# Kernel optimization log

Hardware: AMD Instinct MI355X
Metric: run time of the kernel (lower is better)

The kernel has to match this reference:

```python
import jax, jax.numpy as jnp
import numpy as np

N_U, N_I, D = 30000, 15000, 64
L = 2                 # propagation layers (self.l)
TEMP = 0.2
LAMBDA1, LAMBDA2 = 0.2, 1e-7
H, F = 4, 16          # GAT heads x per-head dim; H*F == D
NEG_SLOPE = 0.2
AVG_DEG = 16
B = 2048


def setup_inputs() -> dict:
    key = jax.random.key(0)
    ks = jax.random.split(key, 10)
    rng = np.random.default_rng(0)
    E_u_0 = jax.random.normal(ks[0], (N_U, D), jnp.float32) * 0.1
    E_i_0 = jax.random.normal(ks[1], (N_I, D), jnp.float32) * 0.1
    # sparse normalized bipartite adjacency (adj_norm) as an edge list
    nnz = N_U * AVG_DEG
    u_idx = np.repeat(np.arange(N_U), AVG_DEG)
    i_idx = rng.integers(0, N_I, nnz)
    deg_u = np.bincount(u_idx, minlength=N_U)
    deg_i = np.maximum(np.bincount(i_idx, minlength=N_I), 1)
    vals = (1.0 / np.sqrt(deg_u[u_idx] * deg_i[i_idx])).astype(np.float32)
    # GAT graph on n_u+n_i nodes: bipartite edges both directions + self-loops
    n = N_U + N_I
    src = np.concatenate([u_idx, i_idx + N_U, np.arange(n)]).astype(np.int32)
    dst = np.concatenate([i_idx + N_U, u_idx, np.arange(n)]).astype(np.int32)
    # GAT parameters (fresh each forward in original, so just random)
    W = jax.random.normal(ks[2], (D, H * F), jnp.float32) / np.sqrt(D)
    attn_l = jax.random.normal(ks[3], (H, F), jnp.float32) * 0.1
    attn_r = jax.random.normal(ks[4], (H, F), jnp.float32) * 0.1
    uids = jax.random.randint(ks[5], (B,), 0, N_U, jnp.int32)
    iids = jax.random.randint(ks[6], (B,), 0, N_I, jnp.int32)
    pos = jax.random.randint(ks[7], (B,), 0, N_I, jnp.int32)
    neg = jax.random.randint(ks[8], (B,), 0, N_I, jnp.int32)
    return dict(E_u_0=E_u_0, E_i_0=E_i_0, adj_vals=jnp.asarray(vals),
                W=W, attn_l=attn_l, attn_r=attn_r,
                u_idx=jnp.asarray(u_idx, jnp.int32), i_idx=jnp.asarray(i_idx, jnp.int32),
                src=jnp.asarray(src), dst=jnp.asarray(dst),
                uids=uids, iids=iids, pos=pos, neg=neg)


def gat_layer(h, src, dst, W, attn_l, attn_r, n_nodes):
    # GATConv: project, per-edge attention, neighborhood softmax, scatter-agg
    feat = (h @ W).reshape(-1, H, F)                      # [N,H,F]
    el = (feat * attn_l).sum(-1)                          # [N,H]
    er = (feat * attn_r).sum(-1)                          # [N,H]
    e = jax.nn.leaky_relu(el[src] + er[dst], NEG_SLOPE)   # [E,H]
    e_max = jax.ops.segment_max(e, dst, num_segments=n_nodes)
    a = jnp.exp(e - e_max[dst])
    denom = jax.ops.segment_sum(a, dst, num_segments=n_nodes)
    a = a / denom[dst]                                    # self-loops => denom>0
    out = jax.ops.segment_sum(a[:, :, None] * feat[src], dst, num_segments=n_nodes)
    return jax.nn.elu(out.reshape(-1, H * F))             # [N,D]


def _forward(E_u_0, E_i_0, adj_vals, W, attn_l, attn_r,
             u_idx, i_idx, src, dst, uids, iids, pos, neg):
    n = N_U + N_I
    Eu, Ei = E_u_0, E_i_0
    sum_Eu, sum_Ei = E_u_0, E_i_0
    sum_Gu, sum_Gi = E_u_0, E_i_0
    for _ in range(L):
        # LightGCN spmm propagation: Z_u = A @ E_i, Z_i = A.T @ E_u
        Zu = jax.ops.segment_sum(adj_vals[:, None] * Ei[i_idx], u_idx, num_segments=N_U)
        Zi = jax.ops.segment_sum(adj_vals[:, None] * Eu[u_idx], i_idx, num_segments=N_I)
        ls1 = gat_layer(jnp.concatenate([Eu, Ei], 0), src, dst, W, attn_l, attn_r, n)
        Gu, Gi = ls1[:N_U], ls1[N_U:]
        Eu, Ei = Zu + Eu, Zi + Ei
        sum_Eu = sum_Eu + Eu
        sum_Ei = sum_Ei + Ei
        sum_Gu = sum_Gu + Gu
        sum_Gi = sum_Gi + Gi
    log_eps = jnp.float32(np.log(1e-8))
    # InfoNCE: log(sum(exp(s)) + 1e-8) == logaddexp(logsumexp(s), log(1e-8))
    lse_u = jax.scipy.special.logsumexp(sum_Gu[uids] @ sum_Eu.T / TEMP, axis=1)
    lse_i = jax.scipy.special.logsumexp(sum_Gi[iids] @ sum_Ei.T / TEMP, axis=1)
    neg_score = jnp.logaddexp(lse_u, log_eps).mean() + jnp.logaddexp(lse_i, log_eps).mean()
    pos_score = ((sum_Gu[uids] * sum_Eu[uids]).sum(1) / TEMP).mean() \
              + ((sum_Gi[iids] * sum_Ei[iids]).sum(1) / TEMP).mean()
    loss_s = -pos_score + neg_score
    # BPR loss
    u_emb = sum_Eu[uids]
    diff = (u_emb * sum_Ei[pos]).sum(-1) - (u_emb * sum_Ei[neg]).sum(-1)
    loss_r = -jax.nn.log_sigmoid(diff).mean()
    # L2 reg over nn.Parameters (E_u_0, E_i_0 only)
    loss_reg = LAMBDA2 * ((E_u_0 ** 2).sum() + (E_i_0 ** 2).sum())
    loss = loss_r + LAMBDA1 * loss_s + loss_reg
    return loss, loss_r, LAMBDA1 * loss_s


def reference(E_u_0, E_i_0, adj_vals, W, attn_l, attn_r,
              u_idx, i_idx, src, dst, uids, iids, pos, neg):
    return _forward(E_u_0, E_i_0, adj_vals, W, attn_l, attn_r,
                    u_idx, i_idx, src, dst, uids, iids, pos, neg)
```

## Files before the change

### kernel.cpp

```cpp
#include <hip/hip_runtime.h>
#include <math.h>

#define N_U 30000
#define N_I 15000
#define N_TOT 45000
#define D 64
#define NNZ 480000
#define B 2048
#define INV_TEMP 5.0f
#define LOG_EPS -18.420680743952367f
#define NEG_SLOPE 0.2f
#define LAMBDA1 0.2f
#define LAMBDA2 1e-7f

#define NSP 128
#define RSP_U 235
#define RSP_I 118
#define PAD_U 30016
#define PAD_I 15040
#define SCALE_LOG2 7.2134752044448170f
#define LN2F 0.6931471805599453f

typedef __attribute__((ext_vector_type(8))) short short8;
typedef __attribute__((ext_vector_type(4))) float f32x4;

__device__ inline float wred(float v) {
#pragma unroll
  for (int o = 32; o > 0; o >>= 1) v += __shfl_down(v, o, 64);
  return v;
}

__device__ inline float leaky(float v) { return (v >= 0.f) ? v : NEG_SLOPE * v; }

__device__ inline void atomMaxF(float* a, float v) {
  if (v >= 0.f) atomicMax((int*)a, __float_as_int(v));
  else atomicMin((unsigned int*)a, __float_as_uint(v));
}

__device__ inline unsigned short f2bf(float x) {
  unsigned u = __float_as_uint(x);
  unsigned r = u + 0x7FFFu + ((u >> 16) & 1u);
  return (unsigned short)(r >> 16);
}
__device__ inline float bf2f(unsigned short h) {
  return __uint_as_float(((unsigned)h) << 16);
}

__global__ void k_init(const float* __restrict__ Eu0, const float* __restrict__ Ei0,
                       float* fU, float* fI,
                       unsigned short* gU, unsigned short* gI,
                       float* sEu, float* sEi,
                       float* sGu, float* sGi, int* deg, float* acc) {
  int t = blockIdx.x * 256 + threadIdx.x;
  if (t < 20) acc[t] = (t >= 8 && t < 16) ? -INFINITY : 0.f;
  if (t < N_I) deg[t] = 0;
  int n = t >> 4, q = t & 15;
  if (n < N_U) {
    float4 v = ((const float4*)Eu0)[t];
    ((float4*)(fU + (size_t)n * 128))[q] = v;
    ushort4 bv = {f2bf(v.x), f2bf(v.y), f2bf(v.z), f2bf(v.w)};
    ((ushort4*)(gU + (size_t)n * 128))[q] = bv;
    ((float4*)sEu)[t] = v;
    ((float4*)sGu)[t] = v;
  } else if (n < N_TOT) {
    int j = t - N_U * 16;
    int ni = n - N_U;
    float4 v = ((const float4*)Ei0)[j];
    ((float4*)(fI + (size_t)ni * 128))[q] = v;
    ushort4 bv = {f2bf(v.x), f2bf(v.y), f2bf(v.z), f2bf(v.w)};
    ((ushort4*)(gI + (size_t)ni * 128))[q] = bv;
    ((float4*)sEi)[j] = v;
    ((float4*)sGi)[j] = v;
  }
}

__global__ void k_deg(const int* __restrict__ ii, int* deg) {
  int e = blockIdx.x * 256 + threadIdx.x;
  if (e < NNZ) atomicAdd(&deg[ii[e]], 1);
}

__global__ void k_scan(const int* __restrict__ deg, int* rowptr, int* cursor) {
  __shared__ int wtot[16], woff[16];
  const int CHUNK = 15;
  int tid = threadIdx.x, lane = tid & 63, wv = tid >> 6;
  int base = tid * CHUNK;
  int dv[CHUNK];
  int s = 0;
#pragma unroll
  for (int k = 0; k < CHUNK; k++) {
    int idx = base + k;
    dv[k] = (idx < N_I) ? deg[idx] : 0;
    s += dv[k];
  }
  int v = s;
#pragma unroll
  for (int o = 1; o < 64; o <<= 1) {
    int x = __shfl_up(v, o, 64);
    if (lane >= o) v += x;
  }
  if (lane == 63) wtot[wv] = v;
  __syncthreads();
  if (tid < 16) {
    int w = wtot[tid];
    int iv = w;
#pragma unroll
    for (int o = 1; o < 16; o <<= 1) {
      int x = __shfl_up(iv, o, 16);
      if (tid >= o) iv += x;
    }
    woff[tid] = iv - w;
  }
  __syncthreads();
  int excl = (v - s) + woff[wv];
#pragma unroll
  for (int k = 0; k < CHUNK; k++) {
    int idx = base + k;
    if (idx < N_I) {
      rowptr[idx] = excl;
      cursor[idx] = excl;
      excl += dv[k];
    }
  }
  if (tid == 1023) rowptr[N_I] = excl;
}

__global__ void k_fill(const int* __restrict__ ii, const float* __restrict__ vals,
                       int* cursor, int* u_srt, float* v_srt) {
  int e = blockIdx.x * 256 + threadIdx.x;
  if (e < NNZ) {
    int pos = atomicAdd(&cursor[ii[e]], 1);
    u_srt[pos] = e >> 4;
    v_srt[pos] = vals[e];
  }
}

__global__ void k_feat(float* __restrict__ fU, float* __restrict__ fI,
                       unsigned short* __restrict__ gU, unsigned short* __restrict__ gI,
                       const float* __restrict__ W, const float* __restrict__ al,
                       const float* __restrict__ ar,
                       float* __restrict__ el, float* __restrict__ er) {
  __shared__ float Ws[64 * 64];
  __shared__ float hs[16][64];
  int tid = threadIdx.x;
  for (int t = tid; t < 1024; t += 256) ((float4*)Ws)[t] = ((const float4*)W)[t];
  int g = tid >> 6, c = tid & 63;
  int n0 = blockIdx.x * 16 + g * 4;
  float* rows[4];
  unsigned short* grows[4];
#pragma unroll
  for (int j = 0; j < 4; j++) {
    int node = n0 + j;
    rows[j] = nullptr; grows[j] = nullptr;
    if (node < N_TOT) {
      if (node < N_U) {
        rows[j] = fU + (size_t)node * 128;
        grows[j] = gU + (size_t)node * 128;
      } else {
        rows[j] = fI + (size_t)(node - N_U) * 128;
        grows[j] = gI + (size_t)(node - N_U) * 128;
      }
      hs[g * 4 + j][c] = rows[j][c];
    }
  }
  __syncthreads();
  float a0 = 0.f, a1 = 0.f, a2 = 0.f, a3 = 0.f;
#pragma unroll 8
  for (int k = 0; k < 64; ++k) {
    float w = Ws[k * 64 + c];
    a0 = fmaf(hs[g * 4 + 0][k], w, a0);
    a1 = fmaf(hs[g * 4 + 1][k], w, a1);
    a2 = fmaf(hs[g * 4 + 2][k], w, a2);
    a3 = fmaf(hs[g * 4 + 3][k], w, a3);
  }
  float accs[4] = {a0, a1, a2, a3};
  float alc = al[c], arc = ar[c];
#pragma unroll
  for (int j = 0; j < 4; j++) {
    int node = n0 + j;
    if (node >= N_TOT) continue;
    rows[j][64 + c] = accs[j];
    grows[j][64 + c] = f2bf(accs[j]);
    float pl = accs[j] * alc;
    float pr = accs[j] * arc;
#pragma unroll
    for (int o = 8; o >= 1; o >>= 1) {
      pl += __shfl_down(pl, o, 16);
      pr += __shfl_down(pr, o, 16);
    }
    if ((c & 15) == 0) {
      el[node * 4 + (c >> 4)] = pl;
      er[node * 4 + (c >> 4)] = pr;
    }
  }
}

__global__ void k_elmax(const float* __restrict__ el, float* __restrict__ dst) {
  __shared__ float red[4][4];
  int tid = threadIdx.x;
  int lane = tid & 63, wv = tid >> 6;
  float mx = -INFINITY;
  for (int t = blockIdx.x * 256 + tid; t < N_TOT * 4; t += 64 * 256)
    mx = fmaxf(mx, el[t]);
#pragma unroll
  for (int o = 4; o < 64; o <<= 1) mx = fmaxf(mx, __shfl_xor(mx, o, 64));
  if (lane < 4) red[wv][lane] = mx;
  __syncthreads();
  if (tid < 4) {
    float m2 = fmaxf(fmaxf(red[0][tid], red[1][tid]), fmaxf(red[2][tid], red[3][tid]));
    atomMaxF(dst + tid, m2);
  }
}

__global__ void k_layer(const float* __restrict__ fU_cur, const float* __restrict__ fI_cur,
                        const unsigned short* __restrict__ gU_cur,
                        const unsigned short* __restrict__ gI_cur,
                        const float* __restrict__ el, const float* __restrict__ er,
                        const float* __restrict__ vals, const int* __restrict__ ii,
                        const int* __restrict__ rowptr, const int* __restrict__ u_srt,
                        const float* __restrict__ v_srt,
                        const float* __restrict__ elmx,
                        float* __restrict__ fU_nxt, float* __restrict__ fI_nxt,
                        unsigned short* __restrict__ gU_nxt, unsigned short* __restrict__ gI_nxt,
                        float* __restrict__ sEu, float* __restrict__ sEi,
                        float* __restrict__ sGu, float* __restrict__ sGi,
                        unsigned short* __restrict__ EuH, unsigned short* __restrict__ EuL,
                        unsigned short* __restrict__ EiH, unsigned short* __restrict__ EiL,
                        float* __restrict__ normU, float* __restrict__ normI) {
  int t = blockIdx.x * 256 + threadIdx.x;
  int node = t >> 6, c = t & 63;
  if (node >= N_TOT) return;
  int h = c >> 4;

  if (node < N_U) {
    int u = node;
    float eru = er[u * 4 + h];
    float m = leaky(elmx[h] + eru);
    const float* selfrow = fU_cur + (size_t)u * 128;
    float aself = __expf(leaky(el[u * 4 + h] + eru) - m);

    int idx[16]; float vv[16];
#pragma unroll
    for (int k = 0; k < 16; k++) { idx[k] = ii[u * 16 + k]; vv[k] = vals[u * 16 + k]; }
    float av[16];
#pragma unroll
    for (int k = 0; k < 16; k++)
      av[k] = __expf(leaky(el[(idx[k] + N_U) * 4 + h] + eru) - m);

    float den = aself;
#pragma unroll
    for (int k = 0; k < 16; k++) den += av[k];

    float o0 = aself * selfrow[64 + c], o1 = 0.f;
    float z0 = 0.f, z1 = 0.f;
#pragma unroll
    for (int k = 0; k < 16; k += 2) {
      const unsigned short* rA = gI_cur + (size_t)idx[k] * 128;
      const unsigned short* rB = gI_cur + (size_t)idx[k + 1] * 128;
      float eA = bf2f(rA[c]), fA = bf2f(rA[64 + c]);
      float eB = bf2f(rB[c]), fB = bf2f(rB[64 + c]);
      z0 = fmaf(vv[k], eA, z0);
      z1 = fmaf(vv[k + 1], eB, z1);
      o0 = fmaf(av[k], fA, o0);
      o1 = fmaf(av[k + 1], fB, o1);
    }
    float o = (o0 + o1) / den;
    float g = (o > 0.f) ? o : expm1f(o);
    float e_new = selfrow[c] + z0 + z1;
    fU_nxt[(size_t)u * 128 + c] = e_new;
    gU_nxt[(size_t)u * 128 + c] = f2bf(e_new);
    size_t off = (size_t)u * D + c;
    float s_final = sEu[off] + e_new;
    sEu[off] = s_final;
    sGu[off] += g;
    if (EuH) {
      unsigned short hi = f2bf(s_final);
      EuH[off] = hi;
      EuL[off] = f2bf(s_final - bf2f(hi));
      float n2 = wred(s_final * s_final);
      if (c == 0) normU[u] = n2;
    }
  } else {
    int i = node - N_U;
    float eri = er[node * 4 + h];
    float m = leaky(elmx[h] + eri);
    const float* selfrow = fI_cur + (size_t)i * 128;
    float aself = __expf(leaky(el[node * 4 + h] + eri) - m);
    float den0 = aself, den1 = 0.f;
    float o0 = aself * selfrow[64 + c], o1 = 0.f;
    float z0 = 0.f, z1 = 0.f;
    int r0 = rowptr[i], r1 = rowptr[i + 1];
    int r = r0;
    for (; r + 3 < r1; r += 4) {
      int u0 = u_srt[r], u1 = u_srt[r + 1], u2 = u_srt[r + 2], u3 = u_srt[r + 3];
      float v0 = v_srt[r], v1 = v_srt[r + 1], v2 = v_srt[r + 2], v3 = v_srt[r + 3];
      float a0 = __expf(leaky(el[u0 * 4 + h] + eri) - m);
      float a1 = __expf(leaky(el[u1 * 4 + h] + eri) - m);
      float a2 = __expf(leaky(el[u2 * 4 + h] + eri) - m);
      float a3 = __expf(leaky(el[u3 * 4 + h] + eri) - m);
      const unsigned short* R0 = gU_cur + (size_t)u0 * 128;
      const unsigned short* R1 = gU_cur + (size_t)u1 * 128;
      const unsigned short* R2 = gU_cur + (size_t)u2 * 128;
      const unsigned short* R3 = gU_cur + (size_t)u3 * 128;
      float e0 = bf2f(R0[c]), f0 = bf2f(R0[64 + c]);
      float e1 = bf2f(R1[c]), f1 = bf2f(R1[64 + c]);
      float e2 = bf2f(R2[c]), f2 = bf2f(R2[64 + c]);
      float e3 = bf2f(R3[c]), f3 = bf2f(R3[64 + c]);
      z0 = fmaf(v0, e0, z0); z1 = fmaf(v1, e1, z1);
      z0 = fmaf(v2, e2, z0); z1 = fmaf(v3, e3, z1);
      den0 += a0 + a2; den1 += a1 + a3;
      o0 = fmaf(a0, f0, o0); o1 = fmaf(a1, f1, o1);
      o0 = fmaf(a2, f2, o0); o1 = fmaf(a3, f3, o1);
    }
    for (; r < r1; r++) {
      int u0 = u_srt[r];
      float v0 = v_srt[r];
      float a0 = __expf(leaky(el[u0 * 4 + h] + eri) - m);
      const unsigned short* R0 = gU_cur + (size_t)u0 * 128;
      float e0 = bf2f(R0[c]), f0 = bf2f(R0[64 + c]);
      z0 = fmaf(v0, e0, z0);
      den0 += a0;
      o0 = fmaf(a0, f0, o0);
    }
    float o = (o0 + o1) / (den0 + den1);
    float g = (o > 0.f) ? o : expm1f(o);
    float e_new = selfrow[c] + z0 + z1;
    fI_nxt[(size_t)i * 128 + c] = e_new;
    gI_nxt[(size_t)i * 128 + c] = f2bf(e_new);
    size_t off = (size_t)i * D + c;
    float s_final = sEi[off] + e_new;
    sEi[off] = s_final;
    sGi[off] += g;
    if (EiH) {
      unsigned short hi = f2bf(s_final);
      EiH[off] = hi;
      EiL[off] = f2bf(s_final - bf2f(hi));
      float n2 = wred(s_final * s_final);
      if (c == 0) normI[i] = n2;
    }
  }
}

__global__ void k_normreg(const float* __restrict__ nU, const float* __restrict__ nI,
                          const float* __restrict__ Eu0, const float* __restrict__ Ei0,
                          float* __restrict__ acc) {
  __shared__ float red[4][3];
  int tid = threadIdx.x;
  int lane = tid & 63, wv = tid >> 6;
  float mu = 0.f, mi = 0.f, s = 0.f;
  for (int t = blockIdx.x * 256 + tid; t < N_U; t += 128 * 256) mu = fmaxf(mu, nU[t]);
  for (int t = blockIdx.x * 256 + tid; t < N_I; t += 128 * 256) mi = fmaxf(mi, nI[t]);
  const float4* A = (const float4*)Eu0;
  const float4* Bp = (const float4*)Ei0;
  const int nA = N_U * 16, nTot = N_TOT * 16;
  for (int t = blockIdx.x * 256 + tid; t < nTot; t += 128 * 256) {
    float4 v = (t < nA) ? A[t] : Bp[t - nA];
    s += v.x * v.x + v.y * v.y + v.z * v.z + v.w * v.w;
  }
#pragma unroll
  for (int o = 32; o > 0; o >>= 1) {
    mu = fmaxf(mu, __shfl_down(mu, o, 64));
    mi = fmaxf(mi, __shfl_down(mi, o, 64));
    s += __shfl_down(s, o, 64);
  }
  if (lane == 0) { red[wv][0] = mu; red[wv][1] = mi; red[wv][2] = s; }
  __syncthreads();
  if (tid == 0) {
    float a = fmaxf(fmaxf(red[0][0], red[1][0]), fmaxf(red[2][0], red[3][0]));
    float b = fmaxf(fmaxf(red[0][1], red[1][1]), fmaxf(red[2][1], red[3][1]));
    float ssum = red[0][2] + red[1][2] + red[2][2] + red[3][2];
    atomMaxF(acc + 6, a);
    atomMaxF(acc + 7, b);
    unsafeAtomicAdd(acc + 5, ssum);
  }
}

__global__ void k_cvt_q(const float* __restrict__ sGu, const float* __restrict__ sGi,
                        const int* __restrict__ uids, const int* __restrict__ iids,
                        unsigned short* __restrict__ QuH, unsigned short* __restrict__ QuL,
                        unsigned short* __restrict__ QiH, unsigned short* __restrict__ QiL,
                        const float* __restrict__ acc,
                        float* __restrict__ M0u, float* __restrict__ M0i) {
  int lane = threadIdx.x & 63, wv = threadIdx.x >> 6;
  int row = blockIdx.x * 4 + wv;
  int side = row >> 11;
  int b = row & (B - 1);
  int id = side ? iids[b] : uids[b];
  float x = (side ? sGi : sGu)[(size_t)id * 64 + lane] * SCALE_LOG2;
  unsigned short hi = f2bf(x);
  unsigned short lo = f2bf(x - bf2f(hi));
  if (side) { QiH[(size_t)b * 64 + lane] = hi; QiL[(size_t)b * 64 + lane] = lo; }
  else      { QuH[(size_t)b * 64 + lane] = hi; QuL[(size_t)b * 64 + lane] = lo; }
  float n2 = wred(x * x);
  if (lane == 0) {
    float en2 = side ? acc[7] : acc[6];
    float M0 = sqrtf(n2) * sqrtf(en2) * 1.01f + 1.0f;
    (side ? M0i : M0u)[b] = M0;
  }
}

__global__ __launch_bounds__(256, 2) void k_lse_mfma(
    const unsigned short* __restrict__ QuH, const unsigned short* __restrict__ QuL,
    const unsigned short* __restrict__ EuHp, const unsigned short* __restrict__ EuLp,
    const unsigned short* __restrict__ QiH, const unsigned short* __restrict__ QiL,
    const unsigned short* __restrict__ EiHp, const unsigned short* __restrict__ EiLp,
    const float* __restrict__ M0u, const float* __restrict__ M0i,
    float* __restrict__ psU, float* __restrict__ psI) {
  int z = blockIdx.z;
  const unsigned short* Qhi = z ? QiH : QuH;
  const unsigned short* Qlo = z ? QiL : QuL;
  const unsigned short* Ehi = z ? EiHp : EuHp;
  const unsigned short* Elo = z ? EiLp : EuLp;
  const float* M0arr = z ? M0i : M0u;
  float* part_s = z ? psI : psU;
  int n_rows = z ? N_I : N_U;
  int rows_per_split = z ? RSP_I : RSP_U;

  int tid = threadIdx.x;
  int wave = tid >> 6, lane = tid & 63;
  int l15 = lane & 15, quad = lane >> 4;
  int qbase = (blockIdx.x * 4 + wave) * 128;
  int split = blockIdx.y;
  int row0 = split * rows_per_split;
  int row_end = min(row0 + rows_per_split, n_rows);
  int rows = row_end - row0; if (rows < 0) rows = 0;
  int total = (rows + 15) >> 4;
  int ntail = rows & 15;

  float ss[8][4];
#pragma unroll
  for (int t = 0; t < 8; t++)
#pragma unroll
    for (int g = 0; g < 4; g++) ss[t][g] = 0.f;

  if (total > 0) {
    short8 ah[8][2], al[8][2];
#pragma unroll
    for (int t = 0; t < 8; t++)
#pragma unroll
      for (int c = 0; c < 2; c++) {
        size_t idx = (size_t)(qbase + t * 16 + l15) * 64 + c * 32 + quad * 8;
        ah[t][c] = *(const short8*)(Qhi + idx);
        al[t][c] = *(const short8*)(Qlo + idx);
      }

    f32x4 cinit[8];
#pragma unroll
    for (int t = 0; t < 8; t++)
#pragma unroll
      for (int g = 0; g < 4; g++)
        cinit[t][g] = -M0arr[qbase + t * 16 + quad * 4 + g];

    const unsigned short* ph = Ehi + (size_t)(row0 + l15) * 64 + quad * 8;
    const unsigned short* pl = Elo + (size_t)(row0 + l15) * 64 + quad * 8;

    short8 cb0 = *(const short8*)(ph);
    short8 cb1 = *(const short8*)(ph + 32);
    short8 cb2 = *(const short8*)(pl);
    short8 cb3 = *(const short8*)(pl + 32);
    ph += 1024; pl += 1024;

    for (int it = 0; it < total - 1; it++) {
      short8 nb0 = *(const short8*)(ph);
      short8 nb1 = *(const short8*)(ph + 32);
      short8 nb2 = *(const short8*)(pl);
      short8 nb3 = *(const short8*)(pl + 32);
      ph += 1024; pl += 1024;
#pragma unroll
      for (int t = 0; t < 8; t++) {
        f32x4 acc = cinit[t];
        acc = __builtin_amdgcn_mfma_f32_16x16x32_bf16(ah[t][0], cb0, acc, 0, 0, 0);
        acc = __builtin_amdgcn_mfma_f32_16x16x32_bf16(ah[t][1], cb1, acc, 0, 0, 0);
        acc = __builtin_amdgcn_mfma_f32_16x16x32_bf16(al[t][0], cb0, acc, 0, 0, 0);
        acc = __builtin_amdgcn_mfma_f32_16x16x32_bf16(al[t][1], cb1, acc, 0, 0, 0);
        acc = __builtin_amdgcn_mfma_f32_16x16x32_bf16(ah[t][0], cb2, acc, 0, 0, 0);
        acc = __builtin_amdgcn_mfma_f32_16x16x32_bf16(ah[t][1], cb3, acc, 0, 0, 0);
#pragma unroll
        for (int g = 0; g < 4; g++)
          ss[t][g] += exp2f(acc[g]);
      }
      cb0 = nb0; cb1 = nb1; cb2 = nb2; cb3 = nb3;
    }
    {
      bool valid = (ntail == 0) || (l15 < ntail);
#pragma unroll
      for (int t = 0; t < 8; t++) {
        f32x4 acc = cinit[t];
        acc = __builtin_amdgcn_mfma_f32_16x16x32_bf16(ah[t][0], cb0, acc, 0, 0, 0);
        acc = __builtin_amdgcn_mfma_f32_16x16x32_bf16(ah[t][1], cb1, acc, 0, 0, 0);
        acc = __builtin_amdgcn_mfma_f32_16x16x32_bf16(al[t][0], cb0, acc, 0, 0, 0);
        acc = __builtin_amdgcn_mfma_f32_16x16x32_bf16(al[t][1], cb1, acc, 0, 0, 0);
        acc = __builtin_amdgcn_mfma_f32_16x16x32_bf16(ah[t][0], cb2, acc, 0, 0, 0);
        acc = __builtin_amdgcn_mfma_f32_16x16x32_bf16(ah[t][1], cb3, acc, 0, 0, 0);
#pragma unroll
        for (int g = 0; g < 4; g++) {
          float e = exp2f(acc[g]);
          ss[t][g] += valid ? e : 0.f;
        }
      }
    }
  }

#pragma unroll
  for (int off = 1; off < 16; off <<= 1) {
#pragma unroll
    for (int t = 0; t < 8; t++)
#pragma unroll
      for (int g = 0; g < 4; g++)
        ss[t][g] += __shfl_xor(ss[t][g], off, 64);
  }

  if (l15 == 0) {
#pragma unroll
    for (int t = 0; t < 8; t++)
#pragma unroll
      for (int g = 0; g < 4; g++) {
        int q = qbase + t * 16 + quad * 4 + g;
        part_s[(size_t)split * B + q] = ss[t][g];
      }
  }
}

__global__ void k_small(const float* __restrict__ sEu, const float* __restrict__ sEi,
                        const float* __restrict__ sGu, const float* __restrict__ sGi,
                        const int* __restrict__ uids, const int* __restrict__ iids,
                        const int* __restrict__ pos, const int* __restrict__ neg,
                        const float* __restrict__ psU, const float* __restrict__ psI,
                        const float* __restrict__ M0u, const float* __restrict__ M0i,
                        float* acc, float* __restrict__ out) {
  int b = blockIdx.x * 256 + threadIdx.x;
  float du = 0.f, di = 0.f, nu = 0.f, ni = 0.f, bpr = 0.f;
  if (b < B) {
    float su = 0.f, si = 0.f;
    for (int s2 = 0; s2 < NSP; s2++) su += psU[(size_t)s2 * B + b];
    for (int s2 = 0; s2 < NSP; s2++) si += psI[(size_t)s2 * B + b];
    float lseu = M0u[b] * LN2F + logf(su);
    float lsei = M0i[b] * LN2F + logf(si);
    nu = fmaxf(lseu, LOG_EPS) + log1pf(expf(-fabsf(lseu - LOG_EPS)));
    ni = fmaxf(lsei, LOG_EPS) + log1pf(expf(-fabsf(lsei - LOG_EPS)));

    int u = uids[b], it = iids[b], p = pos[b], ng = neg[b];
    const float4* gu = (const float4*)(sGu + (size_t)u * D);
    const float4* eu = (const float4*)(sEu + (size_t)u * D);
    const float4* gi = (const float4*)(sGi + (size_t)it * D);
    const float4* ei = (const float4*)(sEi + (size_t)it * D);
    const float4* ep = (const float4*)(sEi + (size_t)p * D);
    const float4* en = (const float4*)(sEi + (size_t)ng * D);
    float diff = 0.f;
#pragma unroll
    for (int k = 0; k < 16; k++) {
      float4 a = gu[k], b4 = eu[k];
      du += a.x * b4.x + a.y * b4.y + a.z * b4.z + a.w * b4.w;
      float4 c = gi[k], d4 = ei[k];
      di += c.x * d4.x + c.y * d4.y + c.z * d4.z + c.w * d4.w;
      float4 e = ep[k], f = en[k];
      diff += b4.x * (e.x - f.x) + b4.y * (e.y - f.y) + b4.z * (e.z - f.z) + b4.w * (e.w - f.w);
    }
    bpr = (diff > 0.f) ? log1pf(expf(-diff)) : (-diff + log1pf(expf(diff)));
  }
  du = wred(du); di = wred(di); nu = wred(nu); ni = wred(ni); bpr = wred(bpr);
  if ((threadIdx.x & 63) == 0) {
    unsafeAtomicAdd(acc + 0, du);
    unsafeAtomicAdd(acc + 1, di);
    unsafeAtomicAdd(acc + 2, nu);
    unsafeAtomicAdd(acc + 3, ni);
    unsafeAtomicAdd(acc + 4, bpr);
  }
  __syncthreads();
  if (threadIdx.x == 0) {
    __threadfence();
    int ticket = atomicAdd((int*)(acc + 16), 1);
    if (ticket == (int)gridDim.x - 1) {
      __threadfence();
      float a0 = unsafeAtomicAdd(acc + 0, 0.f);
      float a1 = unsafeAtomicAdd(acc + 1, 0.f);
      float a2 = unsafeAtomicAdd(acc + 2, 0.f);
      float a3 = unsafeAtomicAdd(acc + 3, 0.f);
      float a4 = unsafeAtomicAdd(acc + 4, 0.f);
      float a5 = unsafeAtomicAdd(acc + 5, 0.f);
      float pos_score = (a0 + a1) * (INV_TEMP / (float)B);
      float neg_score = (a2 + a3) / (float)B;
      float loss_s = neg_score - pos_score;
      float loss_r = a4 / (float)B;
      float reg = LAMBDA2 * a5;
      out[0] = loss_r + LAMBDA1 * loss_s + reg;
      out[1] = loss_r;
      out[2] = LAMBDA1 * loss_s;
    }
  }
}

extern "C" void kernel_launch(void* const* d_in, const int* in_sizes, int n_in,
                              void* d_out, int out_size, void* d_ws, size_t ws_size,
                              hipStream_t stream) {
  const float* Eu0  = (const float*)d_in[0];
  const float* Ei0  = (const float*)d_in[1];
  const float* vals = (const float*)d_in[2];
  const float* W    = (const float*)d_in[3];
  const float* al   = (const float*)d_in[4];
  const float* ar   = (const float*)d_in[5];
  const int* ii     = (const int*)d_in[7];
  const int* uids   = (const int*)d_in[10];
  const int* iids   = (const int*)d_in[11];
  const int* pos    = (const int*)d_in[12];
  const int* neg    = (const int*)d_in[13];
  float* out = (float*)d_out;

  char* base = (char*)d_ws;
  size_t off = 0;
  auto alloc = [&](size_t bytes) -> void* {
    void* p = base + off;
    off = (off + bytes + 255) & ~(size_t)255;
    return p;
  };
  float* fU_a = (float*)alloc((size_t)N_U * 128 * 4);
  float* fU_b = (float*)alloc((size_t)N_U * 128 * 4);
  float* fI_a = (float*)alloc((size_t)N_I * 128 * 4);
  float* fI_b = (float*)alloc((size_t)N_I * 128 * 4);
  unsigned short* gU_a = (unsigned short*)alloc((size_t)N_U * 128 * 2);
  unsigned short* gU_b = (unsigned short*)alloc((size_t)N_U * 128 * 2);
  unsigned short* gI_a = (unsigned short*)alloc((size_t)N_I * 128 * 2);
  unsigned short* gI_b = (unsigned short*)alloc((size_t)N_I * 128 * 2);
  float* sEu  = (float*)alloc((size_t)N_U * D * 4);
  float* sEi  = (float*)alloc((size_t)N_I * D * 4);
  float* sGu  = (float*)alloc((size_t)N_U * D * 4);
  float* sGi  = (float*)alloc((size_t)N_I * D * 4);
  float* el   = (float*)alloc((size_t)N_TOT * 4 * 4);
  float* er   = (float*)alloc((size_t)N_TOT * 4 * 4);
  float* psU  = (float*)alloc((size_t)B * NSP * 4);
  float* psI  = (float*)alloc((size_t)B * NSP * 4);
  float* M0u  = (float*)alloc((size_t)B * 4);
  float* M0i  = (float*)alloc((size_t)B * 4);
  float* normU= (float*)alloc((size_t)N_U * 4);
  float* normI= (float*)alloc((size_t)N_I * 4);
  float* acc  = (float*)alloc(32 * 4);
  int* deg    = (int*)alloc((size_t)N_I * 4);
  int* cursor = (int*)alloc((size_t)N_I * 4);
  int* rowptr = (int*)alloc((size_t)(N_I + 1) * 4);
  int* u_srt  = (int*)alloc((size_t)NNZ * 4);
  float* v_srt= (float*)alloc((size_t)NNZ * 4);
  unsigned short* EuH = (unsigned short*)alloc((size_t)PAD_U * 64 * 2);
  unsigned short* EuL = (unsigned short*)alloc((size_t)PAD_U * 64 * 2);
  unsigned short* EiH = (unsigned short*)alloc((size_t)PAD_I * 64 * 2);
  unsigned short* EiL = (unsigned short*)alloc((size_t)PAD_I * 64 * 2);
  unsigned short* QuH = (unsigned short*)alloc((size_t)B * 64 * 2);
  unsigned short* QuL = (unsigned short*)alloc((size_t)B * 64 * 2);
  unsigned short* QiH = (unsigned short*)alloc((size_t)B * 64 * 2);
  unsigned short* QiL = (unsigned short*)alloc((size_t)B * 64 * 2);

  k_init<<<(N_TOT * 16 + 255) / 256, 256, 0, stream>>>(Eu0, Ei0, fU_a, fI_a, gU_a, gI_a,
                                                       sEu, sEi, sGu, sGi, deg, acc);
  k_deg<<<(NNZ + 255) / 256, 256, 0, stream>>>(ii, deg);
  k_scan<<<1, 1024, 0, stream>>>(deg, rowptr, cursor);
  k_fill<<<(NNZ + 255) / 256, 256, 0, stream>>>(ii, vals, cursor, u_srt, v_srt);

  float* cu = fU_a; float* ci = fI_a;
  float* nu = fU_b; float* ni = fI_b;
  unsigned short* gcu = gU_a; unsigned short* gci = gI_a;
  unsigned short* gnu = gU_b; unsigned short* gni = gI_b;
  for (int l = 0; l < 2; ++l) {
    float* elmx = acc + 8 + 4 * l;
    bool last = (l == 1);
    k_feat<<<(N_TOT + 15) / 16, 256, 0, stream>>>(cu, ci, gcu, gci, W, al, ar, el, er);
    k_elmax<<<64, 256, 0, stream>>>(el, elmx);
    k_layer<<<(N_TOT * D) / 256, 256, 0, stream>>>(
        cu, ci, gcu, gci, el, er, vals, ii, rowptr, u_srt, v_srt, elmx,
        nu, ni, gnu, gni, sEu, sEi, sGu, sGi,
        last ? EuH : nullptr, last ? EuL : nullptr,
        last ? EiH : nullptr, last ? EiL : nullptr,
        normU, normI);
    float* t1 = cu; cu = nu; nu = t1;
    float* t2 = ci; ci = ni; ni = t2;
    unsigned short* t3 = gcu; gcu = gnu; gnu = t3;
    unsigned short* t4 = gci; gci = gni; gni = t4;
  }

  k_normreg<<<128, 256, 0, stream>>>(normU, normI, Eu0, Ei0, acc);
  k_cvt_q<<<(2 * B) / 4, 256, 0, stream>>>(sGu, sGi, uids, iids, QuH, QuL, QiH, QiL, acc, M0u, M0i);
  k_lse_mfma<<<dim3(B / 512, NSP, 2), 256, 0, stream>>>(QuH, QuL, EuH, EuL,
                                                        QiH, QiL, EiH, EiL,
                                                        M0u, M0i, psU, psI);
  k_small<<<B / 256, 256, 0, stream>>>(sEu, sEi, sGu, sGi, uids, iids, pos, neg,
                                       psU, psI, M0u, M0i, acc, out);
}
```

Baseline: 424.7 us.

## Interleave bf16 embedding/feature pairs and compute attention exps once per lane with shuffles

Changes the bf16 gather buffers so that the embedding and the projected GAT feature for each channel sit next to each other, letting one 32-bit load fetch both instead of two 16-bit loads from separate halves of the row. Each lane in a 16-lane head group now computes the attention exp for one neighbour and shares it with the others through wave shuffles, rather than every lane recomputing all 16 exps. The item path is restructured into 16-edge chunks to fit the shuffle scheme. This adds shuffle traffic and a layout dependency between the init, projection and propagate kernels.

After: 409.5 us. 3.6% less time.

```diff
diff --git a/kernel.cpp b/kernel.cpp
--- a/kernel.cpp
+++ b/kernel.cpp
@@ -58,8 +58,8 @@
   if (n < N_U) {
     float4 v = ((const float4*)Eu0)[t];
     ((float4*)(fU + (size_t)n * 128))[q] = v;
-    ushort4 bv = {f2bf(v.x), f2bf(v.y), f2bf(v.z), f2bf(v.w)};
-    ((ushort4*)(gU + (size_t)n * 128))[q] = bv;
+    uint4 gv = {(unsigned)f2bf(v.x), (unsigned)f2bf(v.y), (unsigned)f2bf(v.z), (unsigned)f2bf(v.w)};
+    ((uint4*)(gU + (size_t)n * 128))[q] = gv;
     ((float4*)sEu)[t] = v;
     ((float4*)sGu)[t] = v;
   } else if (n < N_TOT) {
@@ -67,8 +67,8 @@
     int ni = n - N_U;
     float4 v = ((const float4*)Ei0)[j];
     ((float4*)(fI + (size_t)ni * 128))[q] = v;
-    ushort4 bv = {f2bf(v.x), f2bf(v.y), f2bf(v.z), f2bf(v.w)};
-    ((ushort4*)(gI + (size_t)ni * 128))[q] = bv;
+    uint4 gv = {(unsigned)f2bf(v.x), (unsigned)f2bf(v.y), (unsigned)f2bf(v.z), (unsigned)f2bf(v.w)};
+    ((uint4*)(gI + (size_t)ni * 128))[q] = gv;
     ((float4*)sEi)[j] = v;
     ((float4*)sGi)[j] = v;
   }
@@ -179,7 +179,7 @@
     int node = n0 + j;
     if (node >= N_TOT) continue;
     rows[j][64 + c] = accs[j];
-    grows[j][64 + c] = f2bf(accs[j]);
+    grows[j][2 * c + 1] = f2bf(accs[j]);
     float pl = accs[j] * alc;
     float pr = accs[j] * arc;
 #pragma unroll
@@ -230,6 +230,7 @@
   int node = t >> 6, c = t & 63;
   if (node >= N_TOT) return;
   int h = c >> 4;
+  int k2 = c & 15;
 
   if (node < N_U) {
     int u = node;
@@ -241,10 +242,12 @@
     int idx[16]; float vv[16];
 #pragma unroll
     for (int k = 0; k < 16; k++) { idx[k] = ii[u * 16 + k]; vv[k] = vals[u * 16 + k]; }
+
+    float ev = __expf(leaky(el[(ii[u * 16 + k2] + N_U) * 4 + h] + eru) - m);
     float av[16];
 #pragma unroll
     for (int k = 0; k < 16; k++)
-      av[k] = __expf(leaky(el[(idx[k] + N_U) * 4 + h] + eru) - m);
+      av[k] = __shfl(ev, (c & 48) | k, 64);
 
     float den = aself;
 #pragma unroll
@@ -254,10 +257,10 @@
     float z0 = 0.f, z1 = 0.f;
 #pragma unroll
     for (int k = 0; k < 16; k += 2) {
-      const unsigned short* rA = gI_cur + (size_t)idx[k] * 128;
-      const unsigned short* rB = gI_cur + (size_t)idx[k + 1] * 128;
-      float eA = bf2f(rA[c]), fA = bf2f(rA[64 + c]);
-      float eB = bf2f(rB[c]), fB = bf2f(rB[64 + c]);
+      unsigned wA = *(const unsigned*)(gI_cur + (size_t)idx[k] * 128 + 2 * c);
+      unsigned wB = *(const unsigned*)(gI_cur + (size_t)idx[k + 1] * 128 + 2 * c);
+      float eA = __uint_as_float(wA << 16), fA = __uint_as_float(wA & 0xFFFF0000u);
+      float eB = __uint_as_float(wB << 16), fB = __uint_as_float(wB & 0xFFFF0000u);
       z0 = fmaf(vv[k], eA, z0);
       z1 = fmaf(vv[k + 1], eB, z1);
       o0 = fmaf(av[k], fA, o0);
@@ -267,7 +270,7 @@
     float g = (o > 0.f) ? o : expm1f(o);
     float e_new = selfrow[c] + z0 + z1;
     fU_nxt[(size_t)u * 128 + c] = e_new;
-    gU_nxt[(size_t)u * 128 + c] = f2bf(e_new);
+    gU_nxt[(size_t)u * 128 + 2 * c] = f2bf(e_new);
     size_t off = (size_t)u * D + c;
     float s_final = sEu[off] + e_new;
     sEu[off] = s_final;
@@ -289,43 +292,48 @@
     float o0 = aself * selfrow[64 + c], o1 = 0.f;
     float z0 = 0.f, z1 = 0.f;
     int r0 = rowptr[i], r1 = rowptr[i + 1];
-    int r = r0;
-    for (; r + 3 < r1; r += 4) {
-      int u0 = u_srt[r], u1 = u_srt[r + 1], u2 = u_srt[r + 2], u3 = u_srt[r + 3];
-      float v0 = v_srt[r], v1 = v_srt[r + 1], v2 = v_srt[r + 2], v3 = v_srt[r + 3];
-      float a0 = __expf(leaky(el[u0 * 4 + h] + eri) - m);
-      float a1 = __expf(leaky(el[u1 * 4 + h] + eri) - m);
-      float a2 = __expf(leaky(el[u2 * 4 + h] + eri) - m);
-      float a3 = __expf(leaky(el[u3 * 4 + h] + eri) - m);
-      const unsigned short* R0 = gU_cur + (size_t)u0 * 128;
-      const unsigned short* R1 = gU_cur + (size_t)u1 * 128;
-      const unsigned short* R2 = gU_cur + (size_t)u2 * 128;
-      const unsigned short* R3 = gU_cur + (size_t)u3 * 128;
-      float e0 = bf2f(R0[c]), f0 = bf2f(R0[64 + c]);
-      float e1 = bf2f(R1[c]), f1 = bf2f(R1[64 + c]);
-      float e2 = bf2f(R2[c]), f2 = bf2f(R2[64 + c]);
-      float e3 = bf2f(R3[c]), f3 = bf2f(R3[64 + c]);
-      z0 = fmaf(v0, e0, z0); z1 = fmaf(v1, e1, z1);
-      z0 = fmaf(v2, e2, z0); z1 = fmaf(v3, e3, z1);
-      den0 += a0 + a2; den1 += a1 + a3;
-      o0 = fmaf(a0, f0, o0); o1 = fmaf(a1, f1, o1);
-      o0 = fmaf(a2, f2, o0); o1 = fmaf(a3, f3, o1);
-    }
-    for (; r < r1; r++) {
-      int u0 = u_srt[r];
-      float v0 = v_srt[r];
-      float a0 = __expf(leaky(el[u0 * 4 + h] + eri) - m);
-      const unsigned short* R0 = gU_cur + (size_t)u0 * 128;
-      float e0 = bf2f(R0[c]), f0 = bf2f(R0[64 + c]);
-      z0 = fmaf(v0, e0, z0);
-      den0 += a0;
-      o0 = fmaf(a0, f0, o0);
+    for (int rb = r0; rb < r1; rb += 16) {
+      int cnt = min(16, r1 - rb);
+      int rr = rb + (k2 < cnt ? k2 : cnt - 1);
+      float ev = __expf(leaky(el[u_srt[rr] * 4 + h] + eri) - m);
+      int k = 0;
+      for (; k + 3 < cnt; k += 4) {
+        int u0 = u_srt[rb + k], u1 = u_srt[rb + k + 1], u2 = u_srt[rb + k + 2], u3 = u_srt[rb + k + 3];
+        float v0 = v_srt[rb + k], v1 = v_srt[rb + k + 1], v2 = v_srt[rb + k + 2], v3 = v_srt[rb + k + 3];
+        float a0 = __shfl(ev, (c & 48) | k, 64);
+        float a1 = __shfl(ev, (c & 48) | (k + 1), 64);
+        float a2 = __shfl(ev, (c & 48) | (k + 2), 64);
+        float a3 = __shfl(ev, (c & 48) | (k + 3), 64);
+        unsigned w0 = *(const unsigned*)(gU_cur + (size_t)u0 * 128 + 2 * c);
+        unsigned w1 = *(const unsigned*)(gU_cur + (size_t)u1 * 128 + 2 * c);
+        unsigned w2 = *(const unsigned*)(gU_cur + (size_t)u2 * 128 + 2 * c);
+        unsigned w3 = *(const unsigned*)(gU_cur + (size_t)u3 * 128 + 2 * c);
+        float e0 = __uint_as_float(w0 << 16), f0 = __uint_as_float(w0 & 0xFFFF0000u);
+        float e1 = __uint_as_float(w1 << 16), f1 = __uint_as_float(w1 & 0xFFFF0000u);
+        float e2 = __uint_as_float(w2 << 16), f2 = __uint_as_float(w2 & 0xFFFF0000u);
+        float e3 = __uint_as_float(w3 << 16), f3 = __uint_as_float(w3 & 0xFFFF0000u);
+        z0 = fmaf(v0, e0, z0); z1 = fmaf(v1, e1, z1);
+        z0 = fmaf(v2, e2, z0); z1 = fmaf(v3, e3, z1);
+        den0 += a0 + a2; den1 += a1 + a3;
+        o0 = fmaf(a0, f0, o0); o1 = fmaf(a1, f1, o1);
+        o0 = fmaf(a2, f2, o0); o1 = fmaf(a3, f3, o1);
+      }
+      for (; k < cnt; k++) {
+        int u0 = u_srt[rb + k];
+        float v0 = v_srt[rb + k];
+        float a0 = __shfl(ev, (c & 48) | k, 64);
+        unsigned w0 = *(const unsigned*)(gU_cur + (size_t)u0 * 128 + 2 * c);
+        float e0 = __uint_as_float(w0 << 16), f0 = __uint_as_float(w0 & 0xFFFF0000u);
+        z0 = fmaf(v0, e0, z0);
+        den0 += a0;
+        o0 = fmaf(a0, f0, o0);
+      }
     }
     float o = (o0 + o1) / (den0 + den1);
     float g = (o > 0.f) ? o : expm1f(o);
     float e_new = selfrow[c] + z0 + z1;
     fI_nxt[(size_t)i * 128 + c] = e_new;
-    gI_nxt[(size_t)i * 128 + c] = f2bf(e_new);
+    gI_nxt[(size_t)i * 128 + 2 * c] = f2bf(e_new);
     size_t off = (size_t)i * D + c;
     float s_final = sEi[off] + e_new;
     sEi[off] = s_final;
```
